# Performance work log

Hardware: AMD Instinct MI355X
Metric: run time of the kernel (lower is better)

The kernel has to match this reference:

```python
import jax, jax.numpy as jnp
import numpy as np

G, N, D, E, L, OUT = 64, 1024, 128, 16384, 2, 64


def setup_inputs() -> dict:
    key = jax.random.key(0)
    ks = jax.random.split(key, 7)
    input_feature = jax.random.normal(ks[0], (G, N, D), jnp.float32)
    edge_index = jax.random.randint(ks[1], (G, 2, E), 0, N, jnp.int32)
    # GraphConv(D, 1): lin_rel (with bias) applied to aggregated neighbors, lin_root (no bias)
    w_rel = jax.random.normal(ks[2], (L, D), jnp.float32) / np.sqrt(D).astype(np.float32)
    b_rel = jnp.zeros((L,), jnp.float32)
    w_root = jax.random.normal(ks[3], (L, D), jnp.float32) / np.sqrt(D).astype(np.float32)
    # SelectTopK(1, ratio): weight is a [1,1] scalar per layer
    w_sel = jax.random.normal(ks[4], (L,), jnp.float32) + 1.5  # keep away from 0
    W_lin = jax.random.normal(ks[5], (2 * D, OUT), jnp.float32) / np.sqrt(2 * D).astype(np.float32)
    b_lin = jnp.zeros((OUT,), jnp.float32)
    return dict(input_feature=input_feature, edge_index=edge_index, w_rel=w_rel,
                b_rel=b_rel, w_root=w_root, w_sel=w_sel, W_lin=W_lin, b_lin=b_lin)


def _sagpool(x, ei, emask, w_rel, b_rel, w_root, w_sel):
    # x: [g, n, d]; ei: [g, 2, e]; emask: [g, e] bool (invalid edges contribute zero)
    g, n, d = x.shape
    src, dst = ei[:, 0], ei[:, 1]  # [g, e] (source_to_target flow)
    gidx = jnp.arange(g)[:, None]
    # GraphConv attention score (out_channels = 1)
    msg = jnp.take_along_axis(x, src[..., None], axis=1) * emask[..., None].astype(x.dtype)  # [g,e,d]
    agg = jnp.zeros_like(x).at[gidx, dst].add(msg)  # segment-sum over dst, [g,n,d]
    attn = agg @ w_rel + b_rel + x @ w_root  # [g, n]
    # SelectTopK: score = tanh(attn * w / ||w||), then per-graph top-k (k = n//2 since ratio=0.5)
    score = jnp.tanh(attn * (w_sel / jnp.abs(w_sel)))
    k = n // 2
    top_s, perm = jax.lax.top_k(score, k)  # [g, k]
    new_x = jnp.take_along_axis(x, perm[..., None], axis=1) * top_s[..., None]  # [g, k, d]
    # FilterEdges: keep edges with both endpoints selected, remap to new node ids
    new_idx = jnp.full((g, n), -1, jnp.int32).at[gidx, perm].set(
        jnp.broadcast_to(jnp.arange(k, dtype=jnp.int32)[None, :], (g, k)))
    src2 = jnp.take_along_axis(new_idx, src, axis=1)
    dst2 = jnp.take_along_axis(new_idx, dst, axis=1)
    new_mask = emask & (src2 >= 0) & (dst2 >= 0)
    src2 = jnp.where(new_mask, src2, 0)
    dst2 = jnp.where(new_mask, dst2, 0)
    return new_x, jnp.stack([src2, dst2], axis=1), new_mask


def reference(input_feature, edge_index, w_rel, b_rel, w_root, w_sel, W_lin, b_lin):
    x, ei = input_feature, edge_index
    emask = jnp.ones((ei.shape[0], ei.shape[2]), dtype=bool)
    for l in range(L):
        x, ei, emask = _sagpool(x, ei, emask, w_rel[l], b_rel[l], w_root[l], w_sel[l])
    # global_mean_pool || global_max_pool per graph, then Linear(2D -> OUT)
    readout = jnp.concatenate([x.mean(axis=1), x.max(axis=1)], axis=-1)  # [G, 2D]
    return readout @ W_lin + b_lin
```

## Files before the change

### kernel.cpp

```cpp
#include <hip/hip_runtime.h>
#include <stdint.h>

#define NG   64
#define N0   1024
#define N1   512
#define K2   256
#define DD   128
#define NE   16384
#define NOUT 64

__device__ __forceinline__ float waveReduceSum(float v) {
    for (int off = 32; off > 0; off >>= 1) v += __shfl_xor(v, off, 64);
    return v;
}

template<int NN>
__device__ __forceinline__ unsigned long long bitonic_desc(
    unsigned long long key, unsigned long long* lds, int i)
{
    for (int k2 = 2; k2 <= NN; k2 <<= 1) {
        for (int j = k2 >> 1; j > 0; j >>= 1) {
            unsigned long long p;
            if (j >= 64) {
                __syncthreads();
                lds[i] = key;
                __syncthreads();
                p = lds[i ^ j];
            } else {
                p = __shfl_xor(key, j, 64);
            }
            bool keepMax = (((i & k2) == 0) == ((i & j) == 0));
            if (keepMax ? (p > key) : (p < key)) key = p;
        }
    }
    return key;
}

__device__ __forceinline__ unsigned long long make_key(float attnv, float sgn, int i, int nn) {
    float sc = tanhf(attnv * sgn);
    unsigned int u = __float_as_uint(sc);
    u = (u & 0x80000000u) ? ~u : (u | 0x80000000u);
    return ((unsigned long long)u << 32) | (unsigned int)(nn - 1 - i);
}

__global__ __launch_bounds__(256) void dots_all_kernel(
    const float* __restrict__ x,
    const float* __restrict__ w_rel, const float* __restrict__ w_root,
    const float* __restrict__ b_rel,
    float* __restrict__ s_rel1, float* __restrict__ attn1,
    float* __restrict__ s_rel2f, float* __restrict__ s_root2f,
    int totalNodes)
{
    int wave = blockIdx.x * 4 + (threadIdx.x >> 6);
    int lane = threadIdx.x & 63;
    float wr10 = w_rel[lane * 2],       wr11 = w_rel[lane * 2 + 1];
    float wo10 = w_root[lane * 2],      wo11 = w_root[lane * 2 + 1];
    float wr20 = w_rel[DD + lane * 2],  wr21 = w_rel[DD + lane * 2 + 1];
    float wo20 = w_root[DD + lane * 2], wo21 = w_root[DD + lane * 2 + 1];
    float b0 = b_rel[0];
    #pragma unroll
    for (int t = 0; t < 4; ++t) {
        int node = wave * 4 + t;
        if (node >= totalNodes) return;
        const float2 v = *(const float2*)(x + (size_t)node * DD + lane * 2);
        float p1 = waveReduceSum(v.x * wr10 + v.y * wr11);
        float p2 = waveReduceSum(v.x * wo10 + v.y * wo11);
        float p3 = waveReduceSum(v.x * wr20 + v.y * wr21);
        float p4 = waveReduceSum(v.x * wo20 + v.y * wo21);
        if (lane == 0) {
            s_rel1[node]   = p1;
            attn1[node]    = p2 + b0;
            s_rel2f[node]  = p3;
            s_root2f[node] = p4;
        }
    }
}

__global__ __launch_bounds__(1024) void graph1_kernel(
    const float* __restrict__ s_rel1,
    const float* __restrict__ attn1in,
    const float* __restrict__ s_rel2f,
    const float* __restrict__ s_root2f,
    const float* __restrict__ b_rel,
    const float* __restrict__ w_sel,
    const int*   __restrict__ ei,
    int*   __restrict__ perm1,
    float* __restrict__ tops1,
    int*   __restrict__ newidx1,
    float* __restrict__ srel2out,
    float* __restrict__ attn2out)
{
    __shared__ float srel[N0];
    __shared__ float attn[N0];
    __shared__ unsigned long long keys[N0];
    const int g = blockIdx.x, i = threadIdx.x;

    srel[i] = s_rel1[(size_t)g * N0 + i];
    attn[i] = attn1in[(size_t)g * N0 + i];
    __syncthreads();

    const int* base = ei + (size_t)g * 2 * NE;
    {
        int4 s4[4], d4[4];
        #pragma unroll
        for (int it = 0; it < 4; ++it) {
            int eo = (it * 1024 + i) * 4;
            s4[it] = *(const int4*)(base + eo);
            d4[it] = *(const int4*)(base + NE + eo);
        }
        #pragma unroll
        for (int it = 0; it < 4; ++it) {
            atomicAdd(&attn[d4[it].x], srel[s4[it].x]);
            atomicAdd(&attn[d4[it].y], srel[s4[it].y]);
            atomicAdd(&attn[d4[it].z], srel[s4[it].z]);
            atomicAdd(&attn[d4[it].w], srel[s4[it].w]);
        }
    }
    __syncthreads();

    const float sgn = (w_sel[0] >= 0.f) ? 1.f : -1.f;
    unsigned long long key = make_key(attn[i], sgn, i, N0);
    key = bitonic_desc<N0>(key, keys, i);

    int idx = (N0 - 1) - (int)(key & 0xffffffffu);
    unsigned int ku = (unsigned int)(key >> 32);
    unsigned int fb = (ku & 0x80000000u) ? (ku ^ 0x80000000u) : ~ku;
    newidx1[(size_t)g * N0 + idx] = (i < N1) ? i : -1;
    if (i < N1) {
        float t = __uint_as_float(fb);
        perm1[(size_t)g * N1 + i] = idx;
        tops1[(size_t)g * N1 + i] = t;
        srel2out[(size_t)g * N1 + i] = t * s_rel2f[(size_t)g * N0 + idx];
        attn2out[(size_t)g * N1 + i] = t * s_root2f[(size_t)g * N0 + idx] + b_rel[1];
    }
}

__global__ __launch_bounds__(1024) void graph2_readout_kernel(
    const float* __restrict__ x0,
    const int*   __restrict__ ei,
    const int*   __restrict__ newidx1,
    const int*   __restrict__ perm1,
    const float* __restrict__ tops1,
    const float* __restrict__ srel2in,
    const float* __restrict__ attn2in,
    const float* __restrict__ w_sel,
    const float* __restrict__ W_lin,
    const float* __restrict__ b_lin,
    float* __restrict__ out)
{
    __shared__ int   nidx[N0];
    __shared__ float srel[N1];
    __shared__ float attn[N1];
    __shared__ unsigned long long keys[N0];
    __shared__ int   p1l[N1];
    __shared__ float t1l[N1];
    __shared__ int   cn0[K2];
    __shared__ float cs[K2];
    __shared__ float sm[4][DD], mm[4][DD], rr[2 * DD], po[4][NOUT];

    const int g = blockIdx.x, i = threadIdx.x;
    const float* xg = x0 + (size_t)g * N0 * DD;
    nidx[i] = newidx1[(size_t)g * N0 + i];
    if (i < N1) {
        srel[i] = srel2in[(size_t)g * N1 + i];
        attn[i] = attn2in[(size_t)g * N1 + i];
        p1l[i]  = perm1[(size_t)g * N1 + i];
        t1l[i]  = tops1[(size_t)g * N1 + i];
    }
    __syncthreads();

    const int* base = ei + (size_t)g * 2 * NE;
    {
        int4 s4[4], d4[4];
        #pragma unroll
        for (int it = 0; it < 4; ++it) {
            int eo = (it * 1024 + i) * 4;
            s4[it] = *(const int4*)(base + eo);
            d4[it] = *(const int4*)(base + NE + eo);
        }
        #pragma unroll
        for (int it = 0; it < 4; ++it) {
            int s2, d2;
            s2 = nidx[s4[it].x]; d2 = nidx[d4[it].x]; if ((s2 | d2) >= 0) atomicAdd(&attn[d2], srel[s2]);
            s2 = nidx[s4[it].y]; d2 = nidx[d4[it].y]; if ((s2 | d2) >= 0) atomicAdd(&attn[d2], srel[s2]);
            s2 = nidx[s4[it].z]; d2 = nidx[d4[it].z]; if ((s2 | d2) >= 0) atomicAdd(&attn[d2], srel[s2]);
            s2 = nidx[s4[it].w]; d2 = nidx[d4[it].w]; if ((s2 | d2) >= 0) atomicAdd(&attn[d2], srel[s2]);
        }
    }
    __syncthreads();

    {
        const float sgn = (w_sel[1] >= 0.f) ? 1.f : -1.f;
        unsigned long long key = (i < N1) ? make_key(attn[i], sgn, i, N1) : 0ULL;
        key = bitonic_desc<N0>(key, keys, i);
        if (i < K2) {
            int idx = (N1 - 1) - (int)(key & 0xffffffffu);
            unsigned int ku = (unsigned int)(key >> 32);
            unsigned int fb = (ku & 0x80000000u) ? (ku ^ 0x80000000u) : ~ku;
            cn0[i] = p1l[idx];
            cs[i]  = __uint_as_float(fb) * t1l[idx];
        }
    }
    __syncthreads();

    if (i < 512) {
        const int d = i & (DD - 1), q = i >> 7;
        float sum = 0.f, mx = -3.0e38f;
        #pragma unroll 4
        for (int j = q * 64; j < q * 64 + 64; ++j) {
            float v = xg[(size_t)cn0[j] * DD + d] * cs[j];
            sum += v;
            mx = fmaxf(mx, v);
        }
        sm[q][d] = sum; mm[q][d] = mx;
    }
    __syncthreads();
    if (i < DD) {
        rr[i] = (sm[0][i] + sm[1][i] + sm[2][i] + sm[3][i]) * (1.f / 256.f);
    } else if (i < 2 * DD) {
        int dd = i - DD;
        rr[DD + dd] = fmaxf(fmaxf(mm[0][dd], mm[1][dd]), fmaxf(mm[2][dd], mm[3][dd]));
    }
    __syncthreads();
    if (i < 256) {
        int o = i & (NOUT - 1), c = i >> 6;
        float acc = 0.f;
        #pragma unroll
        for (int i2 = 0; i2 < 64; ++i2) {
            int ii = c * 64 + i2;
            acc += rr[ii] * W_lin[ii * NOUT + o];
        }
        po[c][o] = acc;
    }
    __syncthreads();
    if (i < NOUT)
        out[(size_t)g * NOUT + i] =
            b_lin[i] + po[0][i] + po[1][i] + po[2][i] + po[3][i];
}

extern "C" void kernel_launch(void* const* d_in, const int* in_sizes, int n_in,
                              void* d_out, int out_size, void* d_ws, size_t ws_size,
                              hipStream_t stream)
{
    const float* x0     = (const float*)d_in[0];
    const int*   ei     = (const int*)  d_in[1];
    const float* w_rel  = (const float*)d_in[2];
    const float* b_rel  = (const float*)d_in[3];
    const float* w_root = (const float*)d_in[4];
    const float* w_sel  = (const float*)d_in[5];
    const float* W_lin  = (const float*)d_in[6];
    const float* b_lin  = (const float*)d_in[7];
    float* out = (float*)d_out;
    (void)in_sizes; (void)n_in; (void)out_size; (void)ws_size;

    char* ws = (char*)d_ws;
    size_t off = 0;
    auto alloc = [&](size_t bytes) -> void* {
        off = (off + 255) & ~(size_t)255;
        void* p = ws + off;
        off += bytes;
        return p;
    };

    float* s_rel1   = (float*)alloc((size_t)NG * N0 * 4);
    float* attn1    = (float*)alloc((size_t)NG * N0 * 4);
    float* s_rel2f  = (float*)alloc((size_t)NG * N0 * 4);
    float* s_root2f = (float*)alloc((size_t)NG * N0 * 4);
    int*   perm1    = (int*)  alloc((size_t)NG * N1 * 4);
    float* tops1    = (float*)alloc((size_t)NG * N1 * 4);
    int*   newidx1  = (int*)  alloc((size_t)NG * N0 * 4);
    float* srel2    = (float*)alloc((size_t)NG * N1 * 4);
    float* attn2    = (float*)alloc((size_t)NG * N1 * 4);

    dots_all_kernel<<<(NG * N0) / 16, 256, 0, stream>>>(
        x0, w_rel, w_root, b_rel, s_rel1, attn1, s_rel2f, s_root2f, NG * N0);

    graph1_kernel<<<NG, 1024, 0, stream>>>(
        s_rel1, attn1, s_rel2f, s_root2f, b_rel, w_sel, ei,
        perm1, tops1, newidx1, srel2, attn2);

    graph2_readout_kernel<<<NG, 1024, 0, stream>>>(
        x0, ei, newidx1, perm1, tops1, srel2, attn2, w_sel + 0,
        W_lin, b_lin, out);
}
```

Measured before the change: 167.2 us.

## Fuse both graph pooling stages and readout into one kernel

Merges graph1_kernel and graph2_readout_kernel into a single per-graph kernel. Stage-1 results (perm, top scores, new indices, stage-2 scores) now stay in LDS instead of going through global workspace, and edge indices are loaded once into registers and reused for both scatter passes. This removes one kernel launch and the global round-trips between the stages, at the cost of higher LDS use per block and more registers held live across the sort.

```diff
diff --git a/kernel.cpp b/kernel.cpp
--- a/kernel.cpp
+++ b/kernel.cpp
@@ -76,122 +76,89 @@
     }
 }
 
-__global__ __launch_bounds__(1024) void graph1_kernel(
+__global__ __launch_bounds__(1024) void graph_all_kernel(
+    const float* __restrict__ x0,
+    const int*   __restrict__ ei,
     const float* __restrict__ s_rel1,
     const float* __restrict__ attn1in,
     const float* __restrict__ s_rel2f,
     const float* __restrict__ s_root2f,
     const float* __restrict__ b_rel,
     const float* __restrict__ w_sel,
-    const int*   __restrict__ ei,
-    int*   __restrict__ perm1,
-    float* __restrict__ tops1,
-    int*   __restrict__ newidx1,
-    float* __restrict__ srel2out,
-    float* __restrict__ attn2out)
+    const float* __restrict__ W_lin,
+    const float* __restrict__ b_lin,
+    float* __restrict__ out)
 {
     __shared__ float srel[N0];
     __shared__ float attn[N0];
     __shared__ unsigned long long keys[N0];
+    __shared__ int   nidx[N0];
+    __shared__ int   p1l[N1];
+    __shared__ float t1l[N1];
+    __shared__ float srel2[N1];
+    __shared__ float attn2[N1];
+    __shared__ int   cn0[K2];
+    __shared__ float cs[K2];
+    __shared__ float sm[4][DD], mm[4][DD], rr[2 * DD], po[4][NOUT];
+
     const int g = blockIdx.x, i = threadIdx.x;
+    const float* xg = x0 + (size_t)g * N0 * DD;
 
     srel[i] = s_rel1[(size_t)g * N0 + i];
     attn[i] = attn1in[(size_t)g * N0 + i];
-    __syncthreads();
-
-    const int* base = ei + (size_t)g * 2 * NE;
+    int4 s4[4], d4[4];
     {
-        int4 s4[4], d4[4];
+        const int* base = ei + (size_t)g * 2 * NE;
         #pragma unroll
         for (int it = 0; it < 4; ++it) {
             int eo = (it * 1024 + i) * 4;
             s4[it] = *(const int4*)(base + eo);
             d4[it] = *(const int4*)(base + NE + eo);
         }
-        #pragma unroll
-        for (int it = 0; it < 4; ++it) {
-            atomicAdd(&attn[d4[it].x], srel[s4[it].x]);
-            atomicAdd(&attn[d4[it].y], srel[s4[it].y]);
-            atomicAdd(&attn[d4[it].z], srel[s4[it].z]);
-            atomicAdd(&attn[d4[it].w], srel[s4[it].w]);
-        }
-    }
-    __syncthreads();
-
-    const float sgn = (w_sel[0] >= 0.f) ? 1.f : -1.f;
-    unsigned long long key = make_key(attn[i], sgn, i, N0);
-    key = bitonic_desc<N0>(key, keys, i);
-
-    int idx = (N0 - 1) - (int)(key & 0xffffffffu);
-    unsigned int ku = (unsigned int)(key >> 32);
-    unsigned int fb = (ku & 0x80000000u) ? (ku ^ 0x80000000u) : ~ku;
-    newidx1[(size_t)g * N0 + idx] = (i < N1) ? i : -1;
-    if (i < N1) {
-        float t = __uint_as_float(fb);
-        perm1[(size_t)g * N1 + i] = idx;
-        tops1[(size_t)g * N1 + i] = t;
-        srel2out[(size_t)g * N1 + i] = t * s_rel2f[(size_t)g * N0 + idx];
-        attn2out[(size_t)g * N1 + i] = t * s_root2f[(size_t)g * N0 + idx] + b_rel[1];
-    }
-}
-
-__global__ __launch_bounds__(1024) void graph2_readout_kernel(
-    const float* __restrict__ x0,
-    const int*   __restrict__ ei,
-    const int*   __restrict__ newidx1,
-    const int*   __restrict__ perm1,
-    const float* __restrict__ tops1,
-    const float* __restrict__ srel2in,
-    const float* __restrict__ attn2in,
-    const float* __restrict__ w_sel,
-    const float* __restrict__ W_lin,
-    const float* __restrict__ b_lin,
-    float* __restrict__ out)
-{
-    __shared__ int   nidx[N0];
-    __shared__ float srel[N1];
-    __shared__ float attn[N1];
-    __shared__ unsigned long long keys[N0];
-    __shared__ int   p1l[N1];
-    __shared__ float t1l[N1];
-    __shared__ int   cn0[K2];
-    __shared__ float cs[K2];
-    __shared__ float sm[4][DD], mm[4][DD], rr[2 * DD], po[4][NOUT];
-
-    const int g = blockIdx.x, i = threadIdx.x;
-    const float* xg = x0 + (size_t)g * N0 * DD;
-    nidx[i] = newidx1[(size_t)g * N0 + i];
-    if (i < N1) {
-        srel[i] = srel2in[(size_t)g * N1 + i];
-        attn[i] = attn2in[(size_t)g * N1 + i];
-        p1l[i]  = perm1[(size_t)g * N1 + i];
-        t1l[i]  = tops1[(size_t)g * N1 + i];
-    }
-    __syncthreads();
-
-    const int* base = ei + (size_t)g * 2 * NE;
+    }
+    __syncthreads();
+
+    #pragma unroll
+    for (int it = 0; it < 4; ++it) {
+        atomicAdd(&attn[d4[it].x], srel[s4[it].x]);
+        atomicAdd(&attn[d4[it].y], srel[s4[it].y]);
+        atomicAdd(&attn[d4[it].z], srel[s4[it].z]);
+        atomicAdd(&attn[d4[it].w], srel[s4[it].w]);
+    }
+    __syncthreads();
+
     {
-        int4 s4[4], d4[4];
-        #pragma unroll
-        for (int it = 0; it < 4; ++it) {
-            int eo = (it * 1024 + i) * 4;
-            s4[it] = *(const int4*)(base + eo);
-            d4[it] = *(const int4*)(base + NE + eo);
-        }
-        #pragma unroll
-        for (int it = 0; it < 4; ++it) {
-            int s2, d2;
-            s2 = nidx[s4[it].x]; d2 = nidx[d4[it].x]; if ((s2 | d2) >= 0) atomicAdd(&attn[d2], srel[s2]);
-            s2 = nidx[s4[it].y]; d2 = nidx[d4[it].y]; if ((s2 | d2) >= 0) atomicAdd(&attn[d2], srel[s2]);
-            s2 = nidx[s4[it].z]; d2 = nidx[d4[it].z]; if ((s2 | d2) >= 0) atomicAdd(&attn[d2], srel[s2]);
-            s2 = nidx[s4[it].w]; d2 = nidx[d4[it].w]; if ((s2 | d2) >= 0) atomicAdd(&attn[d2], srel[s2]);
-        }
+        const float sgn = (w_sel[0] >= 0.f) ? 1.f : -1.f;
+        const float b1 = b_rel[1];
+        unsigned long long key = make_key(attn[i], sgn, i, N0);
+        key = bitonic_desc<N0>(key, keys, i);
+        int idx = (N0 - 1) - (int)(key & 0xffffffffu);
+        unsigned int ku = (unsigned int)(key >> 32);
+        unsigned int fb = (ku & 0x80000000u) ? (ku ^ 0x80000000u) : ~ku;
+        nidx[idx] = (i < N1) ? i : -1;
+        if (i < N1) {
+            float t = __uint_as_float(fb);
+            p1l[i] = idx;
+            t1l[i] = t;
+            srel2[i] = t * s_rel2f[(size_t)g * N0 + idx];
+            attn2[i] = t * s_root2f[(size_t)g * N0 + idx] + b1;
+        }
+    }
+    __syncthreads();
+
+    #pragma unroll
+    for (int it = 0; it < 4; ++it) {
+        int s2, d2;
+        s2 = nidx[s4[it].x]; d2 = nidx[d4[it].x]; if ((s2 | d2) >= 0) atomicAdd(&attn2[d2], srel2[s2]);
+        s2 = nidx[s4[it].y]; d2 = nidx[d4[it].y]; if ((s2 | d2) >= 0) atomicAdd(&attn2[d2], srel2[s2]);
+        s2 = nidx[s4[it].z]; d2 = nidx[d4[it].z]; if ((s2 | d2) >= 0) atomicAdd(&attn2[d2], srel2[s2]);
+        s2 = nidx[s4[it].w]; d2 = nidx[d4[it].w]; if ((s2 | d2) >= 0) atomicAdd(&attn2[d2], srel2[s2]);
     }
     __syncthreads();
 
     {
         const float sgn = (w_sel[1] >= 0.f) ? 1.f : -1.f;
-        unsigned long long key = (i < N1) ? make_key(attn[i], sgn, i, N1) : 0ULL;
+        unsigned long long key = (i < N1) ? make_key(attn2[i], sgn, i, N1) : 0ULL;
         key = bitonic_desc<N0>(key, keys, i);
         if (i < K2) {
             int idx = (N1 - 1) - (int)(key & 0xffffffffu);
@@ -266,20 +233,11 @@
     float* attn1    = (float*)alloc((size_t)NG * N0 * 4);
     float* s_rel2f  = (float*)alloc((size_t)NG * N0 * 4);
     float* s_root2f = (float*)alloc((size_t)NG * N0 * 4);
-    int*   perm1    = (int*)  alloc((size_t)NG * N1 * 4);
-    float* tops1    = (float*)alloc((size_t)NG * N1 * 4);
-    int*   newidx1  = (int*)  alloc((size_t)NG * N0 * 4);
-    float* srel2    = (float*)alloc((size_t)NG * N1 * 4);
-    float* attn2    = (float*)alloc((size_t)NG * N1 * 4);
 
     dots_all_kernel<<<(NG * N0) / 16, 256, 0, stream>>>(
         x0, w_rel, w_root, b_rel, s_rel1, attn1, s_rel2f, s_root2f, NG * N0);
 
-    graph1_kernel<<<NG, 1024, 0, stream>>>(
-        s_rel1, attn1, s_rel2f, s_root2f, b_rel, w_sel, ei,
-        perm1, tops1, newidx1, srel2, attn2);
-
-    graph2_readout_kernel<<<NG, 1024, 0, stream>>>(
-        x0, ei, newidx1, perm1, tops1, srel2, attn2, w_sel + 0,
+    graph_all_kernel<<<NG, 1024, 0, stream>>>(
+        x0, ei, s_rel1, attn1, s_rel2f, s_root2f, b_rel, w_sel,
         W_lin, b_lin, out);
 }
```

Measured after the change: 164.6 us. No clear change (-1.6%).

## Move edge scatter-adds out of per-graph blocks into grid-wide global-atomic kernels

Applied to the files above, without the earlier changes.

The edge aggregation for both pooling layers moves out of the 64 single-block-per-graph kernels into two standalone scatter kernels. These spread all edges across many blocks and use global atomics into zeroed buffers, which the dots kernel now initialises. The goal is to stop the edge loads and atomics from being serialised on only 64 workgroups, so the whole GPU shares that work. In exchange it adds two kernel launches, global atomic contention, and extra global round-trips for the aggregation buffers.

```diff
diff --git a/kernel.cpp b/kernel.cpp
--- a/kernel.cpp
+++ b/kernel.cpp
@@ -49,10 +49,16 @@
     const float* __restrict__ b_rel,
     float* __restrict__ s_rel1, float* __restrict__ attn1,
     float* __restrict__ s_rel2f, float* __restrict__ s_root2f,
+    float* __restrict__ agg1,
+    float* __restrict__ agg2,
     int totalNodes)
 {
     int wave = blockIdx.x * 4 + (threadIdx.x >> 6);
     int lane = threadIdx.x & 63;
+    int gid = blockIdx.x * 256 + threadIdx.x;
+    if (gid < NG * N0) agg1[gid] = 0.f;
+    if (gid < NG * N1) agg2[gid] = 0.f;
+
     float wr10 = w_rel[lane * 2],       wr11 = w_rel[lane * 2 + 1];
     float wo10 = w_root[lane * 2],      wo11 = w_root[lane * 2 + 1];
     float wr20 = w_rel[DD + lane * 2],  wr21 = w_rel[DD + lane * 2 + 1];
@@ -76,50 +82,44 @@
     }
 }
 
+__global__ __launch_bounds__(256) void scatter1_kernel(
+    const int* __restrict__ ei,
+    const float* __restrict__ s_rel1,
+    float* __restrict__ agg1)
+{
+    int e4 = blockIdx.x * 256 + threadIdx.x;
+    int e  = e4 * 4;
+    int g  = e >> 14, eo = e & (NE - 1);
+    const int* base = ei + (size_t)g * 2 * NE;
+    const int4 s4 = *(const int4*)(base + eo);
+    const int4 d4 = *(const int4*)(base + NE + eo);
+    const float* sr = s_rel1 + (g << 10);
+    float* ag = agg1 + (g << 10);
+    atomicAdd(&ag[d4.x], sr[s4.x]);
+    atomicAdd(&ag[d4.y], sr[s4.y]);
+    atomicAdd(&ag[d4.z], sr[s4.z]);
+    atomicAdd(&ag[d4.w], sr[s4.w]);
+}
+
 __global__ __launch_bounds__(1024) void graph1_kernel(
-    const float* __restrict__ s_rel1,
-    const float* __restrict__ attn1in,
+    const float* __restrict__ attn1,
+    const float* __restrict__ agg1,
     const float* __restrict__ s_rel2f,
     const float* __restrict__ s_root2f,
     const float* __restrict__ b_rel,
     const float* __restrict__ w_sel,
-    const int*   __restrict__ ei,
     int*   __restrict__ perm1,
     float* __restrict__ tops1,
     int*   __restrict__ newidx1,
     float* __restrict__ srel2out,
     float* __restrict__ attn2out)
 {
-    __shared__ float srel[N0];
-    __shared__ float attn[N0];
     __shared__ unsigned long long keys[N0];
     const int g = blockIdx.x, i = threadIdx.x;
 
-    srel[i] = s_rel1[(size_t)g * N0 + i];
-    attn[i] = attn1in[(size_t)g * N0 + i];
-    __syncthreads();
-
-    const int* base = ei + (size_t)g * 2 * NE;
-    {
-        int4 s4[4], d4[4];
-        #pragma unroll
-        for (int it = 0; it < 4; ++it) {
-            int eo = (it * 1024 + i) * 4;
-            s4[it] = *(const int4*)(base + eo);
-            d4[it] = *(const int4*)(base + NE + eo);
-        }
-        #pragma unroll
-        for (int it = 0; it < 4; ++it) {
-            atomicAdd(&attn[d4[it].x], srel[s4[it].x]);
-            atomicAdd(&attn[d4[it].y], srel[s4[it].y]);
-            atomicAdd(&attn[d4[it].z], srel[s4[it].z]);
-            atomicAdd(&attn[d4[it].w], srel[s4[it].w]);
-        }
-    }
-    __syncthreads();
-
+    float attnv = attn1[(size_t)g * N0 + i] + agg1[(size_t)g * N0 + i];
     const float sgn = (w_sel[0] >= 0.f) ? 1.f : -1.f;
-    unsigned long long key = make_key(attn[i], sgn, i, N0);
+    unsigned long long key = make_key(attnv, sgn, i, N0);
     key = bitonic_desc<N0>(key, keys, i);
 
     int idx = (N0 - 1) - (int)(key & 0xffffffffu);
@@ -135,22 +135,39 @@
     }
 }
 
+__global__ __launch_bounds__(256) void scatter2_kernel(
+    const int* __restrict__ ei,
+    const int* __restrict__ newidx1,
+    const float* __restrict__ srel2,
+    float* __restrict__ agg2)
+{
+    int e4 = blockIdx.x * 256 + threadIdx.x;
+    int e  = e4 * 4;
+    int g  = e >> 14, eo = e & (NE - 1);
+    const int* base = ei + (size_t)g * 2 * NE;
+    const int4 s4 = *(const int4*)(base + eo);
+    const int4 d4 = *(const int4*)(base + NE + eo);
+    const int* ni = newidx1 + (g << 10);
+    const float* sr = srel2 + (g << 9);
+    float* ag = agg2 + (g << 9);
+    int s2, d2;
+    s2 = ni[s4.x]; d2 = ni[d4.x]; if ((s2 | d2) >= 0) atomicAdd(&ag[d2], sr[s2]);
+    s2 = ni[s4.y]; d2 = ni[d4.y]; if ((s2 | d2) >= 0) atomicAdd(&ag[d2], sr[s2]);
+    s2 = ni[s4.z]; d2 = ni[d4.z]; if ((s2 | d2) >= 0) atomicAdd(&ag[d2], sr[s2]);
+    s2 = ni[s4.w]; d2 = ni[d4.w]; if ((s2 | d2) >= 0) atomicAdd(&ag[d2], sr[s2]);
+}
+
 __global__ __launch_bounds__(1024) void graph2_readout_kernel(
     const float* __restrict__ x0,
-    const int*   __restrict__ ei,
-    const int*   __restrict__ newidx1,
     const int*   __restrict__ perm1,
     const float* __restrict__ tops1,
-    const float* __restrict__ srel2in,
-    const float* __restrict__ attn2in,
+    const float* __restrict__ attn2b,
+    const float* __restrict__ agg2,
     const float* __restrict__ w_sel,
     const float* __restrict__ W_lin,
     const float* __restrict__ b_lin,
     float* __restrict__ out)
 {
-    __shared__ int   nidx[N0];
-    __shared__ float srel[N1];
-    __shared__ float attn[N1];
     __shared__ unsigned long long keys[N0];
     __shared__ int   p1l[N1];
     __shared__ float t1l[N1];
@@ -160,38 +177,18 @@
 
     const int g = blockIdx.x, i = threadIdx.x;
     const float* xg = x0 + (size_t)g * N0 * DD;
-    nidx[i] = newidx1[(size_t)g * N0 + i];
     if (i < N1) {
-        srel[i] = srel2in[(size_t)g * N1 + i];
-        attn[i] = attn2in[(size_t)g * N1 + i];
-        p1l[i]  = perm1[(size_t)g * N1 + i];
-        t1l[i]  = tops1[(size_t)g * N1 + i];
-    }
-    __syncthreads();
-
-    const int* base = ei + (size_t)g * 2 * NE;
-    {
-        int4 s4[4], d4[4];
-        #pragma unroll
-        for (int it = 0; it < 4; ++it) {
-            int eo = (it * 1024 + i) * 4;
-            s4[it] = *(const int4*)(base + eo);
-            d4[it] = *(const int4*)(base + NE + eo);
-        }
-        #pragma unroll
-        for (int it = 0; it < 4; ++it) {
-            int s2, d2;
-            s2 = nidx[s4[it].x]; d2 = nidx[d4[it].x]; if ((s2 | d2) >= 0) atomicAdd(&attn[d2], srel[s2]);
-            s2 = nidx[s4[it].y]; d2 = nidx[d4[it].y]; if ((s2 | d2) >= 0) atomicAdd(&attn[d2], srel[s2]);
-            s2 = nidx[s4[it].z]; d2 = nidx[d4[it].z]; if ((s2 | d2) >= 0) atomicAdd(&attn[d2], srel[s2]);
-            s2 = nidx[s4[it].w]; d2 = nidx[d4[it].w]; if ((s2 | d2) >= 0) atomicAdd(&attn[d2], srel[s2]);
-        }
-    }
-    __syncthreads();
+        p1l[i] = perm1[(size_t)g * N1 + i];
+        t1l[i] = tops1[(size_t)g * N1 + i];
+    }
 
     {
         const float sgn = (w_sel[1] >= 0.f) ? 1.f : -1.f;
-        unsigned long long key = (i < N1) ? make_key(attn[i], sgn, i, N1) : 0ULL;
+        unsigned long long key = 0ULL;
+        if (i < N1) {
+            float attnv = attn2b[(size_t)g * N1 + i] + agg2[(size_t)g * N1 + i];
+            key = make_key(attnv, sgn, i, N1);
+        }
         key = bitonic_desc<N0>(key, keys, i);
         if (i < K2) {
             int idx = (N1 - 1) - (int)(key & 0xffffffffu);
@@ -266,20 +263,27 @@
     float* attn1    = (float*)alloc((size_t)NG * N0 * 4);
     float* s_rel2f  = (float*)alloc((size_t)NG * N0 * 4);
     float* s_root2f = (float*)alloc((size_t)NG * N0 * 4);
+    float* agg1     = (float*)alloc((size_t)NG * N0 * 4);
+    float* agg2     = (float*)alloc((size_t)NG * N1 * 4);
     int*   perm1    = (int*)  alloc((size_t)NG * N1 * 4);
     float* tops1    = (float*)alloc((size_t)NG * N1 * 4);
     int*   newidx1  = (int*)  alloc((size_t)NG * N0 * 4);
     float* srel2    = (float*)alloc((size_t)NG * N1 * 4);
-    float* attn2    = (float*)alloc((size_t)NG * N1 * 4);
+    float* attn2b   = (float*)alloc((size_t)NG * N1 * 4);
 
     dots_all_kernel<<<(NG * N0) / 16, 256, 0, stream>>>(
-        x0, w_rel, w_root, b_rel, s_rel1, attn1, s_rel2f, s_root2f, NG * N0);
+        x0, w_rel, w_root, b_rel, s_rel1, attn1, s_rel2f, s_root2f,
+        agg1, agg2, NG * N0);
+
+    scatter1_kernel<<<(NG * NE) / 1024, 256, 0, stream>>>(ei, s_rel1, agg1);
 
     graph1_kernel<<<NG, 1024, 0, stream>>>(
-        s_rel1, attn1, s_rel2f, s_root2f, b_rel, w_sel, ei,
-        perm1, tops1, newidx1, srel2, attn2);
+        attn1, agg1, s_rel2f, s_root2f, b_rel, w_sel,
+        perm1, tops1, newidx1, srel2, attn2b);
+
+    scatter2_kernel<<<(NG * NE) / 1024, 256, 0, stream>>>(
+        ei, newidx1, srel2, agg2);
 
     graph2_readout_kernel<<<NG, 1024, 0, stream>>>(
-        x0, ei, newidx1, perm1, tops1, srel2, attn2, w_sel + 0,
-        W_lin, b_lin, out);
-}
+        x0, perm1, tops1, attn2b, agg2, w_sel, W_lin, b_lin, out);
+}
```

New measurement: 186.3 us. +11.4%, slower.
